# Performance work log

Hardware: AMD Instinct MI355X
Metric: run time of the kernel (lower is better)

Reference implementation:

```python
import jax, jax.numpy as jnp
import numpy as np

B, S, V, D, F, NC = 256, 64, 100000, 64, 10, 10  # batch, seq, vocab, emb_dim, n_feats, n_clusters


def setup_inputs() -> dict:
    key = jax.random.key(0)
    ks = jax.random.split(key, 12)
    ids = jax.random.randint(ks[0], (B, S), 0, V)
    emb_table = jax.random.normal(ks[1], (V, D), dtype=jnp.float32) * 0.02
    comb_w1 = jax.random.normal(ks[2], (2 * D, D), dtype=jnp.float32) / np.sqrt(2 * D)
    comb_b1 = jnp.zeros((D,), jnp.float32)
    comb_w2 = jax.random.normal(ks[3], (D, F), dtype=jnp.float32) / np.sqrt(D)
    comb_b2 = jnp.zeros((F,), jnp.float32)
    freq_w1 = jax.random.normal(ks[4], (D + 1, D), dtype=jnp.float32) / np.sqrt(D + 1)
    freq_b1 = jnp.zeros((D,), jnp.float32)
    freq_w2 = jax.random.normal(ks[5], (D, F), dtype=jnp.float32) / np.sqrt(D)
    freq_b2 = jnp.zeros((F,), jnp.float32)
    cluster_centers = jax.random.normal(ks[6], (NC, D), dtype=jnp.float32)
    cat_freq = jnp.ones((V,), jnp.float32)          # category_frequencies buffer
    total_samples = jnp.array(1.0, jnp.float32)     # total_samples buffer
    return dict(category_ids=ids, emb_table=emb_table,
                comb_w1=comb_w1, comb_b1=comb_b1, comb_w2=comb_w2, comb_b2=comb_b2,
                freq_w1=freq_w1, freq_b1=freq_b1, freq_w2=freq_w2, freq_b2=freq_b2,
                cluster_centers=cluster_centers, cat_freq=cat_freq,
                total_samples=total_samples)


def reference(category_ids, emb_table, comb_w1, comb_b1, comb_w2, comb_b2,
              freq_w1, freq_b1, freq_w2, freq_b2, cluster_centers,
              cat_freq, total_samples):
    emb = emb_table[category_ids]                      # [B,S,D]
    # --- pairwise combination features (vectorized over all i<j pairs) ---
    iu, ju = np.triu_indices(S, 1)                     # P = S*(S-1)/2 pairs
    P = iu.shape[0]
    pairs = jnp.concatenate([emb[:, iu], emb[:, ju]], axis=-1)   # [B,P,2D]
    h = jax.nn.relu(jnp.einsum('bpe,ed->bpd', pairs, comb_w1) + comb_b1)
    combo = jnp.einsum('bpd,df->bpf', h, comb_w2) + comb_b2      # [B,P,F]
    combo_sum = combo.sum(axis=1)                      # [B,F]
    # --- frequency features ---
    freqs = cat_freq[category_ids] / total_samples     # [B,S]
    freq_in = jnp.concatenate([emb, freqs[..., None]], axis=-1)  # [B,S,D+1]
    fh = jax.nn.relu(jnp.einsum('bse,ed->bsd', freq_in, freq_w1) + freq_b1)
    freq_feat = jnp.einsum('bsd,df->bsf', fh, freq_w2) + freq_b2  # [B,S,F]
    # --- cluster assignment features (softmax over -euclidean distances) ---
    d2 = (jnp.sum(emb * emb, axis=-1, keepdims=True)
          + jnp.sum(cluster_centers * cluster_centers, axis=-1)
          - 2.0 * jnp.einsum('bsd,cd->bsc', emb, cluster_centers))
    dist = jnp.sqrt(jnp.maximum(d2, 0.0))              # [B,S,NC]
    cluster_feat = jax.nn.softmax(-dist, axis=-1)      # [B,S,F] (F==NC)
    # --- mean over stacked features: freq + P pair feats (broadcast over seq) + cluster ---
    out = (freq_feat + combo_sum[:, None, :] + cluster_feat) / (P + 2)
    return out
```

## Files before the change

### kernel.cpp

```cpp
#include <hip/hip_runtime.h>
#include <math.h>


typedef _Float16 h2 __attribute__((ext_vector_type(2)));
typedef _Float16 h8 __attribute__((ext_vector_type(8)));
typedef float f32x4 __attribute__((ext_vector_type(4)));

constexpr int BATCH = 256;
constexpr int NPAIR = 2016;

constexpr int WT_D   = 0;
constexpr int FF_F   = 0;
constexpr int HS_F   = 640;
constexpr int CS_F   = 704;
constexpr int EMBS_D = 6912;
constexpr int PART_F = 6912;
constexpr int EMBT_D = 9216;
constexpr int FHT_D  = 9216;
constexpr int U2B_D  = 11328;
constexpr int CF_F   = 11328;
constexpr int V2B_D  = 13376;
constexpr int DI_F   = 15424;
constexpr int B1F    = 16064;
constexpr int FB1F   = 16128;
constexpr int FW1LF  = 16192;
constexpr int FQF    = 16256;
constexpr int LDS_DW = 16320;

__device__ __forceinline__ h2 pk2(float a, float b) {
#if __has_builtin(__builtin_amdgcn_cvt_pkrtz)
  auto t = __builtin_amdgcn_cvt_pkrtz(a, b);
  return __builtin_bit_cast(h2, t);
#else
  h2 r; r.x = (_Float16)a; r.y = (_Float16)b; return r;
#endif
}

__device__ __forceinline__ h2 hmax2z(h2 a) {
#if __has_builtin(__builtin_elementwise_max)
  h2 z = {(_Float16)0, (_Float16)0};
  return __builtin_elementwise_max(a, z);
#else
  h2 r;
  r.x = a.x > (_Float16)0 ? a.x : (_Float16)0;
  r.y = a.y > (_Float16)0 ? a.y : (_Float16)0;
  return r;
#endif
}

__device__ __forceinline__ float lane_up1(float v) {
#if __has_builtin(__builtin_amdgcn_update_dpp)
  int r = __builtin_amdgcn_update_dpp(0, __float_as_int(v), 0xF5, 0xF, 0xF, false);
  return __int_as_float(r);
#else
  return __shfl_down(v, 1, 64);
#endif
}

__global__ __launch_bounds__(1024, 4)
void cat_enc_kernel(const int*   __restrict__ ids,
                    const float* __restrict__ emb_table,
                    const float* __restrict__ comb_w1,
                    const float* __restrict__ comb_b1,
                    const float* __restrict__ comb_w2,
                    const float* __restrict__ comb_b2,
                    const float* __restrict__ freq_w1,
                    const float* __restrict__ freq_b1,
                    const float* __restrict__ freq_w2,
                    const float* __restrict__ freq_b2,
                    const float* __restrict__ centers,
                    const float* __restrict__ cat_freq,
                    const float* __restrict__ total_samples,
                    float*       __restrict__ out)
{
  __shared__ __align__(16) unsigned int ldsu[LDS_DW];
  h2*    ldsH = (h2*)ldsu;
  float* ldsf = (float*)ldsu;
  const int tid = threadIdx.x;
  const int b = blockIdx.x, bBase = b * 64;
  const int lane = tid & 63;
  const int wv = __builtin_amdgcn_readfirstlane((int)(tid >> 6));

  for (int e = tid; e < 6144; e += 1024) {
    int k2 = e / 192, n = e - k2 * 192;
    int k = 2 * k2;
    float w0, w1;
    if (n < 64)       { w0 = comb_w1[k * 64 + n];            w1 = comb_w1[(k + 1) * 64 + n]; }
    else if (n < 128) { int m = n - 64;  w0 = comb_w1[(64 + k) * 64 + m]; w1 = comb_w1[(65 + k) * 64 + m]; }
    else              { int m = n - 128; w0 = freq_w1[k * 64 + m];        w1 = freq_w1[(k + 1) * 64 + m]; }
    ldsH[WT_D + n * 36 + k2] = pk2(w0, w1);
  }
  {
    int s = tid >> 4, q = tid & 15;
    int id = ids[bBase + s];
    float4 e4 = *(const float4*)(emb_table + (size_t)id * 64 + q * 4);
    h2 p0 = pk2(e4.x, e4.y), p1 = pk2(e4.z, e4.w);
    ldsH[EMBS_D + s * 36 + q * 2]     = p0;
    ldsH[EMBS_D + s * 36 + q * 2 + 1] = p1;
    ldsH[EMBT_D + (q * 2) * 64 + s]     = p0;
    ldsH[EMBT_D + (q * 2 + 1) * 64 + s] = p1;
  }
  if (tid < 256) {
    int g = tid >> 6, l = tid & 63;
    if (g == 0)      ldsf[B1F + l]   = comb_b1[l];
    else if (g == 1) ldsf[FB1F + l]  = freq_b1[l];
    else if (g == 2) ldsf[FW1LF + l] = freq_w1[64 * 64 + l];
    else             ldsf[FQF + l]   = cat_freq[ids[bBase + l]] / total_samples[0];
  }
  __syncthreads();

  f32x4 acc0 = {0.f, 0.f, 0.f, 0.f}, acc1 = acc0, acc2 = acc0, acc3 = acc0;
  const int fi = lane & 15, fq = lane >> 4;
  if (wv < 12) {
    const int mt = wv & 3, ng = wv >> 2;
    const int arow = (mt * 16 + fi) * 36 + fq * 4;
    h8 a0 = *(const h8*)(ldsu + EMBS_D + arow);
    h8 a1 = *(const h8*)(ldsu + EMBS_D + arow + 16);
#pragma unroll
    for (int t = 0; t < 4; ++t) {
      const int brow = (ng * 64 + t * 16 + fi) * 36 + fq * 4;
      h8 b0 = *(const h8*)(ldsu + WT_D + brow);
      h8 b1 = *(const h8*)(ldsu + WT_D + brow + 16);
      f32x4 acc = (t == 0) ? acc0 : (t == 1) ? acc1 : (t == 2) ? acc2 : acc3;
      acc = __builtin_amdgcn_mfma_f32_16x16x32_f16(a0, b0, acc, 0, 0, 0);
      acc = __builtin_amdgcn_mfma_f32_16x16x32_f16(a1, b1, acc, 0, 0, 0);
      if (t == 0) acc0 = acc; else if (t == 1) acc1 = acc;
      else if (t == 2) acc2 = acc; else acc3 = acc;
    }
  } else {
    const int cb = wv - 12;
    const int s = lane;
    float d0 = 0.f, d1 = 0.f, d2 = 0.f;
    const float* c0 = centers + cb * 64;
    const float* c1 = centers + (cb + 4) * 64;
    const float* c2 = centers + (cb + 8) * 64;
#pragma unroll 8
    for (int k2 = 0; k2 < 32; ++k2) {
      h2 e2 = ldsH[EMBT_D + k2 * 64 + s];
      float e0 = (float)e2.x, e1 = (float)e2.y;
      float t0 = e0 - c0[2 * k2], t1 = e1 - c0[2 * k2 + 1];
      d0 = fmaf(t0, t0, fmaf(t1, t1, d0));
      t0 = e0 - c1[2 * k2]; t1 = e1 - c1[2 * k2 + 1];
      d1 = fmaf(t0, t0, fmaf(t1, t1, d1));
      if (cb < 2) {
        t0 = e0 - c2[2 * k2]; t1 = e1 - c2[2 * k2 + 1];
        d2 = fmaf(t0, t0, fmaf(t1, t1, d2));
      }
    }
    ldsf[DI_F + s * 10 + cb]     = sqrtf(d0);
    ldsf[DI_F + s * 10 + cb + 4] = sqrtf(d1);
    if (cb < 2) ldsf[DI_F + s * 10 + cb + 8] = sqrtf(d2);
  }
  __syncthreads();

  if (wv < 12) {
    const int mt = wv & 3, ng = wv >> 2;
    const bool even = ((lane & 1) == 0);
#pragma unroll
    for (int t = 0; t < 4; ++t) {
      const int col = t * 16 + fi;
      f32x4 acc = (t == 0) ? acc0 : (t == 1) ? acc1 : (t == 2) ? acc2 : acc3;
      float bias = 0.f, fb = 0.f, fw = 0.f;
      if (ng == 0)      bias = ldsf[B1F + col];
      else if (ng == 2) { fb = ldsf[FB1F + col]; fw = ldsf[FW1LF + col]; }
#pragma unroll
      for (int r = 0; r < 4; ++r) {
        const int srow = mt * 16 + fq * 4 + r;
        float v = acc[r];
        if (ng == 0)      v += bias;
        else if (ng == 2) v = fmaxf(v + fb + ldsf[FQF + srow] * fw, 0.f);
        float vn = lane_up1(v);
        if (even) {
          const int d2i = col >> 1;
          if (ng == 0)      ldsH[U2B_D + srow * 32 + d2i] = pk2(v, vn);
          else if (ng == 1) ldsH[V2B_D + srow * 32 + d2i] = pk2(v, vn);
          else              ldsH[FHT_D + srow * 33 + d2i] = pk2(v, vn);
        }
      }
    }
  }
  __syncthreads();

  if (tid < 640) {
    const int s = tid & 63;
    const int f = __builtin_amdgcn_readfirstlane((int)(tid >> 6));
    float acc = freq_b2[f];
#pragma unroll 8
    for (int d2i = 0; d2i < 32; ++d2i) {
      h2 fh = ldsH[FHT_D + s * 33 + d2i];
      acc = fmaf((float)fh.x, freq_w2[(2 * d2i) * 10 + f], acc);
      acc = fmaf((float)fh.y, freq_w2[(2 * d2i + 1) * 10 + f], acc);
    }
    ldsf[FF_F + s * 10 + f] = acc;
  }
  {
    const int dg = tid & 31, g = tid >> 5;
    h2 u2a = ldsH[U2B_D + g * 32 + dg];
    h2 u2b = ldsH[U2B_D + (63 - g) * 32 + dg];
    h2 za = {(_Float16)0, (_Float16)0};
    h2 acca = za, accb = za;
    const int jsplit = 64 - g;
#pragma unroll 4
    for (int j = g + 1; j < 64; ++j) {
      h2 v2 = ldsH[V2B_D + j * 32 + dg];
      acca = acca + hmax2z(u2a + v2);
      if (j >= jsplit) accb = accb + hmax2z(u2b + v2);
    }
    h2 at = acca + accb;
    ldsf[PART_F + g * 64 + 2 * dg]     = (float)at.x;
    ldsf[PART_F + g * 64 + 2 * dg + 1] = (float)at.y;
  }
  __syncthreads();

  if (tid < 64) {
    float h = 0.f;
#pragma unroll
    for (int g = 0; g < 32; ++g) h += ldsf[PART_F + g * 64 + tid];
    ldsf[HS_F + tid] = h;
  } else if (tid < 128) {
    const int s = tid - 64;
    float dv[10], dmin = 1e30f;
#pragma unroll
    for (int c = 0; c < 10; ++c) { dv[c] = ldsf[DI_F + s * 10 + c]; dmin = fminf(dmin, dv[c]); }
    float p[10], sum = 0.f;
#pragma unroll
    for (int c = 0; c < 10; ++c) { p[c] = expf(dmin - dv[c]); sum += p[c]; }
    float rs = 1.0f / sum;
#pragma unroll
    for (int c = 0; c < 10; ++c) ldsf[CF_F + s * 10 + c] = p[c] * rs;
  }
  __syncthreads();

  if (tid < 10) {
    float cs = comb_b2[tid] * (float)NPAIR;
#pragma unroll 8
    for (int dd = 0; dd < 64; ++dd)
      cs = fmaf(ldsf[HS_F + dd], comb_w2[dd * 10 + tid], cs);
    ldsf[CS_F + tid] = cs;
  }
  __syncthreads();

  if (tid < 640) {
    const int f = tid % 10;
    float val = (ldsf[FF_F + tid] + ldsf[CS_F + f] + ldsf[CF_F + tid])
              * (1.0f / (float)(NPAIR + 2));
    out[(size_t)b * 640 + tid] = val;
  }
}

extern "C" void kernel_launch(void* const* d_in, const int* in_sizes, int n_in,
                              void* d_out, int out_size, void* d_ws, size_t ws_size,
                              hipStream_t stream) {
  (void)in_sizes; (void)n_in; (void)d_ws; (void)ws_size; (void)out_size;
  const int*   ids        = (const int*)  d_in[0];
  const float* emb_table  = (const float*)d_in[1];
  const float* comb_w1    = (const float*)d_in[2];
  const float* comb_b1    = (const float*)d_in[3];
  const float* comb_w2    = (const float*)d_in[4];
  const float* comb_b2    = (const float*)d_in[5];
  const float* freq_w1    = (const float*)d_in[6];
  const float* freq_b1    = (const float*)d_in[7];
  const float* freq_w2    = (const float*)d_in[8];
  const float* freq_b2    = (const float*)d_in[9];
  const float* centers    = (const float*)d_in[10];
  const float* cat_freq   = (const float*)d_in[11];
  const float* total_samp = (const float*)d_in[12];
  float* out = (float*)d_out;

  hipLaunchKernelGGL(cat_enc_kernel, dim3(BATCH), dim3(1024), 0, stream,
                     ids, emb_table, comb_w1, comb_b1, comb_w2, comb_b2,
                     freq_w1, freq_b1, freq_w2, freq_b2, centers, cat_freq,
                     total_samp, out);
}
```

Baseline: 113.4 us.

## Prepack weights in setup kernel, compute cluster distances via MFMA, rebalance phases

```diff
diff --git a/kernel.cpp b/kernel.cpp
--- a/kernel.cpp
+++ b/kernel.cpp
@@ -3,29 +3,34 @@
 
 
 typedef _Float16 h2 __attribute__((ext_vector_type(2)));
+typedef _Float16 h4 __attribute__((ext_vector_type(4)));
 typedef _Float16 h8 __attribute__((ext_vector_type(8)));
 typedef float f32x4 __attribute__((ext_vector_type(4)));
 
 constexpr int BATCH = 256;
-constexpr int NPAIR = 2016;
+
+constexpr int WS_WT  = 0;
+constexpr int WS_C2  = 6656;
+constexpr int WS_W2P = 6672;
 
 constexpr int WT_D   = 0;
-constexpr int FF_F   = 0;
-constexpr int HS_F   = 640;
-constexpr int CS_F   = 704;
-constexpr int EMBS_D = 6912;
-constexpr int PART_F = 6912;
-constexpr int EMBT_D = 9216;
-constexpr int FHT_D  = 9216;
-constexpr int U2B_D  = 11328;
-constexpr int CF_F   = 11328;
-constexpr int V2B_D  = 13376;
-constexpr int DI_F   = 15424;
-constexpr int B1F    = 16064;
-constexpr int FB1F   = 16128;
-constexpr int FW1LF  = 16192;
-constexpr int FQF    = 16256;
-constexpr int LDS_DW = 16320;
+constexpr int PART_F = 0;
+constexpr int FF_F   = 2048;
+constexpr int CF_F   = 2688;
+constexpr int DI_F   = 3328;
+constexpr int EMBS_D = 7488;
+constexpr int FHT_D  = 7488;
+constexpr int U2B_D  = 9792;
+constexpr int V2B_D  = 11840;
+constexpr int E2_F   = 13888;
+constexpr int B1F    = 13952;
+constexpr int FB1F   = 14016;
+constexpr int FW1L_F = 14080;
+constexpr int FQ_F   = 14144;
+constexpr int W2P_D  = 14208;
+constexpr int C2_F   = 14528;
+constexpr int CS_F   = 14544;
+constexpr int LDS_DW = 14560;
 
 __device__ __forceinline__ h2 pk2(float a, float b) {
 #if __has_builtin(__builtin_amdgcn_cvt_pkrtz)
@@ -57,20 +62,49 @@
 #endif
 }
 
+__global__ __launch_bounds__(256)
+void setup_kernel(const float* __restrict__ comb_w1,
+                  const float* __restrict__ freq_w1,
+                  const float* __restrict__ centers,
+                  const float* __restrict__ freq_w2,
+                  unsigned int* __restrict__ ws)
+{
+  int g = blockIdx.x * 256 + threadIdx.x;
+  if (g < 6656) {
+    int n = g >> 5, k2 = g & 31, k = 2 * k2;
+    float w0, w1;
+    if (n < 64)       { w0 = comb_w1[k * 64 + n];      w1 = comb_w1[(k + 1) * 64 + n]; }
+    else if (n < 128) { int m = n - 64;  w0 = comb_w1[(64 + k) * 64 + m]; w1 = comb_w1[(65 + k) * 64 + m]; }
+    else if (n < 192) { int m = n - 128; w0 = freq_w1[k * 64 + m];        w1 = freq_w1[(k + 1) * 64 + m]; }
+    else { int c = n - 192;
+           w0 = (c < 10) ? centers[c * 64 + k] : 0.f;
+           w1 = (c < 10) ? centers[c * 64 + k + 1] : 0.f; }
+    ws[WS_WT + g] = __builtin_bit_cast(unsigned int, pk2(w0, w1));
+  } else if (g < 6672) {
+    int c = g - 6656;
+    float acc = 0.f;
+    if (c < 10)
+      for (int k = 0; k < 64; ++k) { float v = centers[c * 64 + k]; acc = fmaf(v, v, acc); }
+    ((float*)ws)[WS_C2 + c] = acc;
+  } else if (g < 6992) {
+    int i = g - 6672, d2 = i / 10, f = i - d2 * 10;
+    ws[WS_W2P + i] = __builtin_bit_cast(unsigned int,
+                       pk2(freq_w2[(2 * d2) * 10 + f], freq_w2[(2 * d2 + 1) * 10 + f]));
+  }
+}
+
 __global__ __launch_bounds__(1024, 4)
 void cat_enc_kernel(const int*   __restrict__ ids,
                     const float* __restrict__ emb_table,
-                    const float* __restrict__ comb_w1,
                     const float* __restrict__ comb_b1,
                     const float* __restrict__ comb_w2,
                     const float* __restrict__ comb_b2,
                     const float* __restrict__ freq_w1,
                     const float* __restrict__ freq_b1,
-                    const float* __restrict__ freq_w2,
                     const float* __restrict__ freq_b2,
-                    const float* __restrict__ centers,
                     const float* __restrict__ cat_freq,
                     const float* __restrict__ total_samples,
+                    const unsigned int* __restrict__ ws,
                     float*       __restrict__ out)
 {
   __shared__ __align__(16) unsigned int ldsu[LDS_DW];
@@ -81,144 +115,135 @@
   const int lane = tid & 63;
   const int wv = __builtin_amdgcn_readfirstlane((int)(tid >> 6));
 
-  for (int e = tid; e < 6144; e += 1024) {
-    int k2 = e / 192, n = e - k2 * 192;
-    int k = 2 * k2;
-    float w0, w1;
-    if (n < 64)       { w0 = comb_w1[k * 64 + n];            w1 = comb_w1[(k + 1) * 64 + n]; }
-    else if (n < 128) { int m = n - 64;  w0 = comb_w1[(64 + k) * 64 + m]; w1 = comb_w1[(65 + k) * 64 + m]; }
-    else              { int m = n - 128; w0 = freq_w1[k * 64 + m];        w1 = freq_w1[(k + 1) * 64 + m]; }
-    ldsH[WT_D + n * 36 + k2] = pk2(w0, w1);
+  for (int t = tid; t < 1664; t += 1024) {
+    int row = t >> 3, c4 = t & 7;
+    uint4 v = ((const uint4*)ws)[row * 8 + c4];
+    *(uint4*)(ldsu + WT_D + row * 36 + c4 * 4) = v;
   }
   {
     int s = tid >> 4, q = tid & 15;
     int id = ids[bBase + s];
     float4 e4 = *(const float4*)(emb_table + (size_t)id * 64 + q * 4);
-    h2 p0 = pk2(e4.x, e4.y), p1 = pk2(e4.z, e4.w);
-    ldsH[EMBS_D + s * 36 + q * 2]     = p0;
-    ldsH[EMBS_D + s * 36 + q * 2 + 1] = p1;
-    ldsH[EMBT_D + (q * 2) * 64 + s]     = p0;
-    ldsH[EMBT_D + (q * 2 + 1) * 64 + s] = p1;
-  }
-  if (tid < 256) {
-    int g = tid >> 6, l = tid & 63;
-    if (g == 0)      ldsf[B1F + l]   = comb_b1[l];
-    else if (g == 1) ldsf[FB1F + l]  = freq_b1[l];
-    else if (g == 2) ldsf[FW1LF + l] = freq_w1[64 * 64 + l];
-    else             ldsf[FQF + l]   = cat_freq[ids[bBase + l]] / total_samples[0];
-  }
+    float p = e4.x * e4.x + e4.y * e4.y + e4.z * e4.z + e4.w * e4.w;
+    p += __shfl_xor(p, 1, 64); p += __shfl_xor(p, 2, 64);
+    p += __shfl_xor(p, 4, 64); p += __shfl_xor(p, 8, 64);
+    ldsH[EMBS_D + s * 36 + 2 * q]     = pk2(e4.x, e4.y);
+    ldsH[EMBS_D + s * 36 + 2 * q + 1] = pk2(e4.z, e4.w);
+    if (q == 0) ldsf[E2_F + s] = p;
+  }
+  if (tid < 64)       ldsf[B1F + tid] = comb_b1[tid];
+  else if (tid < 128) ldsf[FB1F + (tid - 64)] = freq_b1[tid - 64];
+  else if (tid < 192) ldsf[FW1L_F + (tid - 128)] = freq_w1[64 * 64 + (tid - 128)];
+  else if (tid < 256) { int l = tid - 192;
+                        ldsf[FQ_F + l] = cat_freq[ids[bBase + l]] / total_samples[0]; }
+  else if (tid < 576) ldsu[W2P_D + (tid - 256)] = ws[WS_W2P + (tid - 256)];
+  else if (tid < 592) ldsf[C2_F + (tid - 576)] = ((const float*)ws)[WS_C2 + (tid - 576)];
   __syncthreads();
 
   f32x4 acc0 = {0.f, 0.f, 0.f, 0.f}, acc1 = acc0, acc2 = acc0, acc3 = acc0;
   const int fi = lane & 15, fq = lane >> 4;
   if (wv < 12) {
-    const int mt = wv & 3, ng = wv >> 2;
-    const int arow = (mt * 16 + fi) * 36 + fq * 4;
-    h8 a0 = *(const h8*)(ldsu + EMBS_D + arow);
-    h8 a1 = *(const h8*)(ldsu + EMBS_D + arow + 16);
-#pragma unroll
-    for (int t = 0; t < 4; ++t) {
-      const int brow = (ng * 64 + t * 16 + fi) * 36 + fq * 4;
-      h8 b0 = *(const h8*)(ldsu + WT_D + brow);
-      h8 b1 = *(const h8*)(ldsu + WT_D + brow + 16);
-      f32x4 acc = (t == 0) ? acc0 : (t == 1) ? acc1 : (t == 2) ? acc2 : acc3;
+    const int brow = WT_D + (wv * 16 + fi) * 36 + fq * 4;
+    h8 b0 = *(const h8*)(ldsu + brow);
+    h8 b1 = *(const h8*)(ldsu + brow + 16);
+#pragma unroll
+    for (int m = 0; m < 4; ++m) {
+      const int arow = EMBS_D + (m * 16 + fi) * 36 + fq * 4;
+      h8 a0 = *(const h8*)(ldsu + arow);
+      h8 a1 = *(const h8*)(ldsu + arow + 16);
+      f32x4 acc = (m == 0) ? acc0 : (m == 1) ? acc1 : (m == 2) ? acc2 : acc3;
       acc = __builtin_amdgcn_mfma_f32_16x16x32_f16(a0, b0, acc, 0, 0, 0);
       acc = __builtin_amdgcn_mfma_f32_16x16x32_f16(a1, b1, acc, 0, 0, 0);
-      if (t == 0) acc0 = acc; else if (t == 1) acc1 = acc;
-      else if (t == 2) acc2 = acc; else acc3 = acc;
+      if (m == 0) acc0 = acc; else if (m == 1) acc1 = acc;
+      else if (m == 2) acc2 = acc; else acc3 = acc;
     }
   } else {
-    const int cb = wv - 12;
-    const int s = lane;
-    float d0 = 0.f, d1 = 0.f, d2 = 0.f;
-    const float* c0 = centers + cb * 64;
-    const float* c1 = centers + (cb + 4) * 64;
-    const float* c2 = centers + (cb + 8) * 64;
-#pragma unroll 8
-    for (int k2 = 0; k2 < 32; ++k2) {
-      h2 e2 = ldsH[EMBT_D + k2 * 64 + s];
-      float e0 = (float)e2.x, e1 = (float)e2.y;
-      float t0 = e0 - c0[2 * k2], t1 = e1 - c0[2 * k2 + 1];
-      d0 = fmaf(t0, t0, fmaf(t1, t1, d0));
-      t0 = e0 - c1[2 * k2]; t1 = e1 - c1[2 * k2 + 1];
-      d1 = fmaf(t0, t0, fmaf(t1, t1, d1));
-      if (cb < 2) {
-        t0 = e0 - c2[2 * k2]; t1 = e1 - c2[2 * k2 + 1];
-        d2 = fmaf(t0, t0, fmaf(t1, t1, d2));
-      }
-    }
-    ldsf[DI_F + s * 10 + cb]     = sqrtf(d0);
-    ldsf[DI_F + s * 10 + cb + 4] = sqrtf(d1);
-    if (cb < 2) ldsf[DI_F + s * 10 + cb + 8] = sqrtf(d2);
+    const int brow = WT_D + (192 + fi) * 36 + fq * 4;
+    h8 b0 = *(const h8*)(ldsu + brow);
+    h8 b1 = *(const h8*)(ldsu + brow + 16);
+    const int m = wv - 12;
+    const int arow = EMBS_D + (m * 16 + fi) * 36 + fq * 4;
+    h8 a0 = *(const h8*)(ldsu + arow);
+    h8 a1 = *(const h8*)(ldsu + arow + 16);
+    acc0 = __builtin_amdgcn_mfma_f32_16x16x32_f16(a0, b0, acc0, 0, 0, 0);
+    acc0 = __builtin_amdgcn_mfma_f32_16x16x32_f16(a1, b1, acc0, 0, 0, 0);
   }
   __syncthreads();
 
   if (wv < 12) {
-    const int mt = wv & 3, ng = wv >> 2;
     const bool even = ((lane & 1) == 0);
 #pragma unroll
-    for (int t = 0; t < 4; ++t) {
-      const int col = t * 16 + fi;
-      f32x4 acc = (t == 0) ? acc0 : (t == 1) ? acc1 : (t == 2) ? acc2 : acc3;
-      float bias = 0.f, fb = 0.f, fw = 0.f;
-      if (ng == 0)      bias = ldsf[B1F + col];
-      else if (ng == 2) { fb = ldsf[FB1F + col]; fw = ldsf[FW1LF + col]; }
+    for (int m = 0; m < 4; ++m) {
+      f32x4 acc = (m == 0) ? acc0 : (m == 1) ? acc1 : (m == 2) ? acc2 : acc3;
 #pragma unroll
       for (int r = 0; r < 4; ++r) {
-        const int srow = mt * 16 + fq * 4 + r;
+        const int srow = m * 16 + fq * 4 + r;
+        const int col = wv * 16 + fi;
         float v = acc[r];
-        if (ng == 0)      v += bias;
-        else if (ng == 2) v = fmaxf(v + fb + ldsf[FQF + srow] * fw, 0.f);
+        if (wv < 4)       v += ldsf[B1F + col];
+        else if (wv >= 8) v = fmaxf(v + ldsf[FB1F + (col - 128)]
+                                     + ldsf[FQ_F + srow] * ldsf[FW1L_F + (col - 128)], 0.f);
         float vn = lane_up1(v);
         if (even) {
-          const int d2i = col >> 1;
-          if (ng == 0)      ldsH[U2B_D + srow * 32 + d2i] = pk2(v, vn);
-          else if (ng == 1) ldsH[V2B_D + srow * 32 + d2i] = pk2(v, vn);
-          else              ldsH[FHT_D + srow * 33 + d2i] = pk2(v, vn);
+          if (wv < 4)      ldsH[U2B_D + srow * 32 + (col >> 1)] = pk2(v, vn);
+          else if (wv < 8) ldsH[V2B_D + srow * 32 + ((col - 64) >> 1)] = pk2(v, vn);
+          else             ldsH[FHT_D + srow * 33 + ((col - 128) >> 1)] = pk2(v, vn);
         }
       }
     }
+  } else if (fi < 10) {
+    const int m = wv - 12;
+#pragma unroll
+    for (int r = 0; r < 4; ++r) {
+      const int s = m * 16 + fq * 4 + r;
+      float d2v = ldsf[E2_F + s] + ldsf[C2_F + fi] - 2.f * acc0[r];
+      ldsf[DI_F + s * 10 + fi] = sqrtf(fmaxf(d2v, 0.f));
+    }
   }
   __syncthreads();
 
-  if (tid < 640) {
-    const int s = tid & 63;
-    const int f = __builtin_amdgcn_readfirstlane((int)(tid >> 6));
-    float acc = freq_b2[f];
-#pragma unroll 8
-    for (int d2i = 0; d2i < 32; ++d2i) {
-      h2 fh = ldsH[FHT_D + s * 33 + d2i];
-      acc = fmaf((float)fh.x, freq_w2[(2 * d2i) * 10 + f], acc);
-      acc = fmaf((float)fh.y, freq_w2[(2 * d2i + 1) * 10 + f], acc);
-    }
-    ldsf[FF_F + s * 10 + f] = acc;
-  }
-  {
-    const int dg = tid & 31, g = tid >> 5;
-    h2 u2a = ldsH[U2B_D + g * 32 + dg];
-    h2 u2b = ldsH[U2B_D + (63 - g) * 32 + dg];
-    h2 za = {(_Float16)0, (_Float16)0};
-    h2 acca = za, accb = za;
+  if (tid < 512) {
+    const int g = tid >> 4, t = tid & 15;
+    h4 uA = *(const h4*)&ldsH[U2B_D + g * 32 + 2 * t];
+    h4 uB = *(const h4*)&ldsH[U2B_D + (63 - g) * 32 + 2 * t];
+    h2 uA0 = {uA.x, uA.y}, uA1 = {uA.z, uA.w};
+    h2 uB0 = {uB.x, uB.y}, uB1 = {uB.z, uB.w};
+    h2 z = {(_Float16)0, (_Float16)0};
+    h2 aA0 = z, aA1 = z, aB0 = z, aB1 = z;
     const int jsplit = 64 - g;
 #pragma unroll 4
     for (int j = g + 1; j < 64; ++j) {
-      h2 v2 = ldsH[V2B_D + j * 32 + dg];
-      acca = acca + hmax2z(u2a + v2);
-      if (j >= jsplit) accb = accb + hmax2z(u2b + v2);
-    }
-    h2 at = acca + accb;
-    ldsf[PART_F + g * 64 + 2 * dg]     = (float)at.x;
-    ldsf[PART_F + g * 64 + 2 * dg + 1] = (float)at.y;
-  }
-  __syncthreads();
-
-  if (tid < 64) {
-    float h = 0.f;
-#pragma unroll
-    for (int g = 0; g < 32; ++g) h += ldsf[PART_F + g * 64 + tid];
-    ldsf[HS_F + tid] = h;
-  } else if (tid < 128) {
-    const int s = tid - 64;
+      h4 vv = *(const h4*)&ldsH[V2B_D + j * 32 + 2 * t];
+      h2 v0 = {vv.x, vv.y}, v1 = {vv.z, vv.w};
+      aA0 = aA0 + hmax2z(uA0 + v0);
+      aA1 = aA1 + hmax2z(uA1 + v1);
+      if (j >= jsplit) {
+        aB0 = aB0 + hmax2z(uB0 + v0);
+        aB1 = aB1 + hmax2z(uB1 + v1);
+      }
+    }
+    h2 t0 = aA0 + aB0, t1 = aA1 + aB1;
+    float4 pw = make_float4((float)t0.x, (float)t0.y, (float)t1.x, (float)t1.y);
+    *(float4*)(ldsf + PART_F + g * 64 + 4 * t) = pw;
+  } else if (tid < 960) {
+    const int task = tid - 512;
+#pragma unroll
+    for (int pass = 0; pass < 2; ++pass) {
+      const int o = task + pass * 448;
+      if (o < 640) {
+        const int s = o / 10, f = o - s * 10;
+        float acc = freq_b2[f];
+#pragma unroll 8
+        for (int d2 = 0; d2 < 32; ++d2) {
+          h2 fh = ldsH[FHT_D + s * 33 + d2];
+          h2 w  = ldsH[W2P_D + d2 * 10 + f];
+          acc += (float)fh.x * (float)w.x + (float)fh.y * (float)w.y;
+        }
+        ldsf[FF_F + o] = acc;
+      }
+    }
+  } else {
+    const int s = tid - 960;
     float dv[10], dmin = 1e30f;
 #pragma unroll
     for (int c = 0; c < 10; ++c) { dv[c] = ldsf[DI_F + s * 10 + c]; dmin = fminf(dmin, dv[c]); }
@@ -231,27 +256,33 @@
   }
   __syncthreads();
 
-  if (tid < 10) {
-    float cs = comb_b2[tid] * (float)NPAIR;
+  if (tid < 64) {
+    float hs = 0.f;
+#pragma unroll
+    for (int g = 0; g < 32; ++g) hs += ldsf[PART_F + g * 64 + tid];
+    ldsf[E2_F + tid] = hs;
+    if (tid < 10) {
+      float cs = comb_b2[tid] * 2016.f;
 #pragma unroll 8
-    for (int dd = 0; dd < 64; ++dd)
-      cs = fmaf(ldsf[HS_F + dd], comb_w2[dd * 10 + tid], cs);
-    ldsf[CS_F + tid] = cs;
-  }
-  __syncthreads();
-
-  if (tid < 640) {
-    const int f = tid % 10;
-    float val = (ldsf[FF_F + tid] + ldsf[CS_F + f] + ldsf[CF_F + tid])
-              * (1.0f / (float)(NPAIR + 2));
-    out[(size_t)b * 640 + tid] = val;
+      for (int d = 0; d < 64; ++d)
+        cs = fmaf(ldsf[E2_F + d], comb_w2[d * 10 + tid], cs);
+      ldsf[CS_F + tid] = cs;
+    }
+    const float inv = 1.0f / 2018.f;
+#pragma unroll
+    for (int m = 0; m < 10; ++m) {
+      const int idx = tid + 64 * m;
+      const int f = idx % 10;
+      float val = (ldsf[FF_F + idx] + ldsf[CS_F + f] + ldsf[CF_F + idx]) * inv;
+      out[(size_t)b * 640 + idx] = val;
+    }
   }
 }
 
 extern "C" void kernel_launch(void* const* d_in, const int* in_sizes, int n_in,
                               void* d_out, int out_size, void* d_ws, size_t ws_size,
                               hipStream_t stream) {
-  (void)in_sizes; (void)n_in; (void)d_ws; (void)ws_size; (void)out_size;
+  (void)in_sizes; (void)n_in; (void)ws_size; (void)out_size;
   const int*   ids        = (const int*)  d_in[0];
   const float* emb_table  = (const float*)d_in[1];
   const float* comb_w1    = (const float*)d_in[2];
@@ -266,9 +297,11 @@
   const float* cat_freq   = (const float*)d_in[11];
   const float* total_samp = (const float*)d_in[12];
   float* out = (float*)d_out;
-
+  unsigned int* ws = (unsigned int*)d_ws;
+
+  hipLaunchKernelGGL(setup_kernel, dim3(28), dim3(256), 0, stream,
+                     comb_w1, freq_w1, centers, freq_w2, ws);
   hipLaunchKernelGGL(cat_enc_kernel, dim3(BATCH), dim3(1024), 0, stream,
-                     ids, emb_table, comb_w1, comb_b1, comb_w2, comb_b2,
-                     freq_w1, freq_b1, freq_w2, freq_b2, centers, cat_freq,
-                     total_samp, out);
-}
+                     ids, emb_table, comb_b1, comb_w2, comb_b2,
+                     freq_w1, freq_b1, freq_b2, cat_freq, total_samp, ws, out);
+}
```

After: 108.1 us. 4.6% less time.
